# Performance work log

Measured on AMD Instinct MI355X. Metric: run time of the kernel, lower is better.

Reference implementation:

```python
import jax, jax.numpy as jnp
import numpy as np

N_NODES = 50000
N_EDGES = 800000
IN_DIM = 128
HID_DIM = 128
OUT_DIM = 128
NUM_GRAPHS = 64
NUM_CLASSES = 3


def _glorot(key, shape):
    lim = np.sqrt(6.0 / (shape[0] + shape[1])).astype(np.float32)
    return jax.random.uniform(key, shape, jnp.float32, -lim, lim)


def setup_inputs() -> dict:
    key = jax.random.key(0)
    ks = jax.random.split(key, 10)
    x = jax.random.normal(ks[0], (N_NODES, IN_DIM), jnp.float32)
    edge_index = jax.random.randint(ks[1], (2, N_EDGES), 0, N_NODES, jnp.int32).astype(jnp.int64)
    batch = jnp.sort(jax.random.randint(ks[2], (N_NODES,), 0, NUM_GRAPHS, jnp.int32)).astype(jnp.int64)
    return {
        "x": x,
        "edge_index": edge_index,
        "batch": batch,
        "W1": _glorot(ks[3], (IN_DIM, HID_DIM)),  "b1": jnp.zeros((HID_DIM,), jnp.float32),
        "W2": _glorot(ks[4], (HID_DIM, HID_DIM)), "b2": jnp.zeros((HID_DIM,), jnp.float32),
        "W3": _glorot(ks[5], (HID_DIM, OUT_DIM)), "b3": jnp.zeros((OUT_DIM,), jnp.float32),
        "C1": _glorot(ks[6], (OUT_DIM, HID_DIM)), "bc1": jnp.zeros((HID_DIM,), jnp.float32),
        "C2": _glorot(ks[7], (HID_DIM, NUM_CLASSES)), "bc2": jnp.zeros((NUM_CLASSES,), jnp.float32),
    }


def _gcn_conv(x, src, dst, norm, W, b):
    # PyG GCNConv: linear transform, then normalized gather/scatter aggregation, then bias.
    h = x @ W                               # [N, F_out]
    msg = h[src] * norm[:, None]            # [E+N, F_out] irregular gather
    return jax.ops.segment_sum(msg, dst, num_segments=N_NODES) + b


def reference(x, edge_index, batch, W1, b1, W2, b2, W3, b3, C1, bc1, C2, bc2):
    loops = jnp.arange(N_NODES, dtype=edge_index.dtype)
    src = jnp.concatenate([edge_index[0], loops])  # add self-loops as in GCNConv
    dst = jnp.concatenate([edge_index[1], loops])
    deg = jax.ops.segment_sum(jnp.ones_like(dst, jnp.float32), dst, num_segments=N_NODES)
    dinv = jnp.where(deg > 0, jax.lax.rsqrt(deg), 0.0)
    norm = dinv[src] * dinv[dst]            # symmetric D^-1/2 (A+I) D^-1/2 weights

    # dropout(p=0.2) is identity at inference time
    h = jax.nn.relu(_gcn_conv(x, src, dst, norm, W1, b1))
    h = jax.nn.relu(_gcn_conv(h, src, dst, norm, W2, b2))
    h = _gcn_conv(h, src, dst, norm, W3, b3)

    # global mean pool over batch segment ids
    counts = jax.ops.segment_sum(jnp.ones((N_NODES,), jnp.float32), batch, num_segments=NUM_GRAPHS)
    pooled = jax.ops.segment_sum(h, batch, num_segments=NUM_GRAPHS) / jnp.maximum(counts, 1.0)[:, None]

    g = jax.nn.relu(pooled @ C1 + bc1)      # classifier MLP (dropout 0.3 inactive)
    return g @ C2 + bc2                     # [NUM_GRAPHS, 3]
```

## Files before the change

kernel.cpp:

```cpp
#include <hip/hip_runtime.h>
#include <hip/hip_bf16.h>

#define N_NODES    50000
#define DIM        128
#define NUM_GRAPHS 64
#define NUM_CLASSES 3
#define NPAD       50176
#define XPITCH     136

typedef unsigned short ushort_t;
typedef unsigned int   uint_t;
typedef __attribute__((ext_vector_type(8))) short short8;
typedef __attribute__((ext_vector_type(4))) float f32x4;

__device__ __forceinline__ ushort_t f2bf(float f) {
    union { float f; uint_t u; } v; v.f = f;
    uint_t r = v.u + 0x7fffu + ((v.u >> 16) & 1u);
    return (ushort_t)(r >> 16);
}
__device__ __forceinline__ float bflo(uint_t u) {
    union { uint_t u; float f; } v; v.u = u << 16; return v.f;
}
__device__ __forceinline__ float bfhi(uint_t u) {
    union { uint_t u; float f; } v; v.u = u & 0xffff0000u; return v.f;
}

__device__ __forceinline__ void gather_raw(
    int n, int lane, const int* __restrict__ rowptr,
    const int* __restrict__ csr_src, const uint_t* __restrict__ Tb,
    float2& acc)
{
    int p0 = rowptr[n], p1 = rowptr[n + 1];
    uint_t us = Tb[n * 64 + lane];
    float2 a0 = make_float2(bflo(us), bfhi(us));
    float2 a1 = make_float2(0.f, 0.f);
    int p = p0;
    int nb = (p1 - p0) >> 3;
    if (nb > 0) {
        uint_t ucur[8];
        #pragma unroll
        for (int q = 0; q < 8; ++q) ucur[q] = Tb[csr_src[p + q] * 64 + lane];
        for (int b = 1; b < nb; ++b) {
            uint_t unxt[8];
            #pragma unroll
            for (int q = 0; q < 8; ++q) unxt[q] = Tb[csr_src[p + 8 + q] * 64 + lane];
            #pragma unroll
            for (int q = 0; q < 8; q += 2) {
                a0.x += bflo(ucur[q]);     a0.y += bfhi(ucur[q]);
                a1.x += bflo(ucur[q + 1]); a1.y += bfhi(ucur[q + 1]);
            }
            #pragma unroll
            for (int q = 0; q < 8; ++q) ucur[q] = unxt[q];
            p += 8;
        }
        #pragma unroll
        for (int q = 0; q < 8; q += 2) {
            a0.x += bflo(ucur[q]);     a0.y += bfhi(ucur[q]);
            a1.x += bflo(ucur[q + 1]); a1.y += bfhi(ucur[q + 1]);
        }
        p += 8;
    }
    for (; p + 4 <= p1; p += 4) {
        int s[4]; uint_t u[4];
        #pragma unroll
        for (int q = 0; q < 4; ++q) s[q] = csr_src[p + q];
        #pragma unroll
        for (int q = 0; q < 4; ++q) u[q] = Tb[s[q] * 64 + lane];
        #pragma unroll
        for (int q = 0; q < 4; q += 2) {
            a0.x += bflo(u[q]);     a0.y += bfhi(u[q]);
            a1.x += bflo(u[q + 1]); a1.y += bfhi(u[q + 1]);
        }
    }
    for (; p < p1; ++p) {
        int s = csr_src[p];
        uint_t u = Tb[s * 64 + lane];
        a0.x += bflo(u); a0.y += bfhi(u);
    }
    acc.x += a0.x + a1.x;
    acc.y += a0.y + a1.y;
}

__global__ void k_init(int* degi, float* pooled, float* counts) {
    int i = blockIdx.x * 256 + threadIdx.x;
    if (i < NPAD) degi[i] = 0;
    if (i < NUM_GRAPHS * DIM) pooled[i] = 0.0f;
    if (i < NUM_GRAPHS) counts[i] = 0.0f;
}

__global__ void k_prep(const float* __restrict__ W1, const float* __restrict__ W2,
                       const float* __restrict__ W3, ushort_t* __restrict__ Wt) {
    int i = blockIdx.x * 256 + threadIdx.x;
    int mat = i >> 14;
    int idx = i & 16383;
    const float* W = (mat == 0) ? W1 : (mat == 1) ? W2 : W3;
    int n = idx >> 7, k = idx & 127;
    Wt[mat * 16384 + n * 128 + k] = f2bf(W[k * 128 + n]);
}

__global__ void k_count(const int* __restrict__ dst, int* degi, int* rank, int nedges) {
    int e = blockIdx.x * 256 + threadIdx.x;
    if (e < nedges) rank[e] = atomicAdd(&degi[dst[e]], 1);
}

__global__ __launch_bounds__(256) void k_scan1(const int* __restrict__ degi,
                                               int* rowptr, int* bsum) {
    __shared__ int sh[256];
    int i = blockIdx.x * 256 + threadIdx.x;
    int v = degi[i];
    sh[threadIdx.x] = v;
    __syncthreads();
    for (int off = 1; off < 256; off <<= 1) {
        int t = (threadIdx.x >= off) ? sh[threadIdx.x - off] : 0;
        __syncthreads();
        sh[threadIdx.x] += t;
        __syncthreads();
    }
    rowptr[i] = sh[threadIdx.x] - v;
    if (threadIdx.x == 255) bsum[blockIdx.x] = sh[255];
}

__global__ __launch_bounds__(256) void k_scan2(int* bsum, int nblocks) {
    __shared__ int sh[256];
    int v = (threadIdx.x < nblocks) ? bsum[threadIdx.x] : 0;
    sh[threadIdx.x] = v;
    __syncthreads();
    for (int off = 1; off < 256; off <<= 1) {
        int t = (threadIdx.x >= off) ? sh[threadIdx.x - off] : 0;
        __syncthreads();
        sh[threadIdx.x] += t;
        __syncthreads();
    }
    if (threadIdx.x < nblocks) bsum[threadIdx.x] = sh[threadIdx.x] - v;
}

__global__ __launch_bounds__(256) void k_scan3(int* rowptr, const int* __restrict__ bsum,
                                               const int* __restrict__ degi,
                                               float* dinv) {
    int i = blockIdx.x * 256 + threadIdx.x;
    rowptr[i] = rowptr[i] + bsum[blockIdx.x];
    if (i < N_NODES) dinv[i] = rsqrtf((float)degi[i] + 1.0f);
}

__global__ void k_fill(const int* __restrict__ src, const int* __restrict__ dst,
                       const int* __restrict__ rank, const int* __restrict__ rowptr,
                       int* csr_src, int nedges) {
    int e = blockIdx.x * 256 + threadIdx.x;
    if (e < nedges) csr_src[rowptr[dst[e]] + rank[e]] = src[e];
}

__global__ __launch_bounds__(256) void k_mm1(
    const float* __restrict__ xin, const ushort_t* __restrict__ WtG,
    const float* __restrict__ dinv, ushort_t* __restrict__ TbOut)
{
    __shared__ ushort_t Wl[DIM * XPITCH];
    __shared__ ushort_t Xl[64 * XPITCH];

    const int tid = threadIdx.x;
    const int rowbase = blockIdx.x * 64;

    #pragma unroll
    for (int i = 0; i < 8; ++i) {
        int g = tid + i * 256;
        uint4 v = ((const uint4*)WtG)[g];
        *((uint4*)&Wl[(g >> 4) * XPITCH + (g & 15) * 8]) = v;
    }
    #pragma unroll
    for (int i = 0; i < 8; ++i) {
        int c = tid + i * 256;
        int row = c >> 5;
        int grow = rowbase + row;
        float4 f = make_float4(0.f, 0.f, 0.f, 0.f);
        if (grow < N_NODES)
            f = ((const float4*)xin)[(long long)rowbase * 32 + c];
        ushort4 h;
        h.x = f2bf(f.x); h.y = f2bf(f.y); h.z = f2bf(f.z); h.w = f2bf(f.w);
        *((ushort4*)&Xl[row * XPITCH + (c & 31) * 4]) = h;
    }
    __syncthreads();

    const int wave = tid >> 6;
    const int lane = tid & 63;
    const int quad = lane >> 4;
    const int lm   = lane & 15;
    const int m0   = wave * 16;

    short8 af[4];
    #pragma unroll
    for (int k0 = 0; k0 < 4; ++k0)
        af[k0] = *(const short8*)&Xl[(m0 + lm) * XPITCH + k0 * 32 + quad * 8];

    int noder[4]; float di[4]; bool okr[4];
    #pragma unroll
    for (int r = 0; r < 4; ++r) {
        noder[r] = rowbase + m0 + quad * 4 + r;
        okr[r] = (noder[r] < N_NODES);
        di[r] = okr[r] ? dinv[noder[r]] : 0.f;
    }

    for (int n0 = 0; n0 < DIM; n0 += 16) {
        f32x4 acc = {0.f, 0.f, 0.f, 0.f};
        #pragma unroll
        for (int k0 = 0; k0 < 4; ++k0) {
            short8 bf = *(const short8*)&Wl[(n0 + lm) * XPITCH + k0 * 32 + quad * 8];
            acc = __builtin_amdgcn_mfma_f32_16x16x32_bf16(af[k0], bf, acc, 0, 0, 0);
        }
        int n = n0 + lm;
        #pragma unroll
        for (int r = 0; r < 4; ++r)
            if (okr[r])
                TbOut[(long long)noder[r] * DIM + n] = f2bf(acc[r] * di[r]);
    }
}

__global__ __launch_bounds__(256) void k_fused(
    const int* __restrict__ rowptr, const int* __restrict__ csr_src,
    const float* __restrict__ dinv, const uint_t* __restrict__ TbIn,
    const ushort_t* __restrict__ WtG, const float* __restrict__ b_prev,
    ushort_t* __restrict__ TbOut)
{
    __shared__ ushort_t Xl[16 * XPITCH];

    const int tid = threadIdx.x;
    const int rowbase = blockIdx.x * 16;
    const int wave = tid >> 6;
    const int lane = tid & 63;

    float2 bias2 = ((const float2*)b_prev)[lane];

    #pragma unroll
    for (int t = 0; t < 4; ++t) {
        int r = wave * 4 + t;
        int n = rowbase + r;
        float2 acc = make_float2(0.f, 0.f);
        float dd = 0.f;
        if (n < N_NODES) {
            dd = dinv[n];
            gather_raw(n, lane, rowptr, csr_src, TbIn, acc);
        }
        ushort2 h;
        h.x = f2bf(fmaxf(bias2.x + acc.x * dd, 0.f));
        h.y = f2bf(fmaxf(bias2.y + acc.y * dd, 0.f));
        *((ushort2*)&Xl[r * XPITCH + lane * 2]) = h;
    }
    __syncthreads();

    const int quad = lane >> 4;
    const int lm   = lane & 15;

    short8 af[4];
    #pragma unroll
    for (int k0 = 0; k0 < 4; ++k0)
        af[k0] = *(const short8*)&Xl[lm * XPITCH + k0 * 32 + quad * 8];

    int noder[4]; float di[4]; bool okr[4];
    #pragma unroll
    for (int r = 0; r < 4; ++r) {
        noder[r] = rowbase + quad * 4 + r;
        okr[r] = (noder[r] < N_NODES);
        di[r] = okr[r] ? dinv[noder[r]] : 0.f;
    }

    #pragma unroll
    for (int h = 0; h < 2; ++h) {
        int n0 = wave * 32 + h * 16;
        f32x4 acc = {0.f, 0.f, 0.f, 0.f};
        #pragma unroll
        for (int k0 = 0; k0 < 4; ++k0) {
            short8 bf = *(const short8*)&WtG[(n0 + lm) * DIM + k0 * 32 + quad * 8];
            acc = __builtin_amdgcn_mfma_f32_16x16x32_bf16(af[k0], bf, acc, 0, 0, 0);
        }
        int n = n0 + lm;
        #pragma unroll
        for (int r = 0; r < 4; ++r)
            if (okr[r])
                TbOut[(long long)noder[r] * DIM + n] = f2bf(acc[r] * di[r]);
    }
}

__global__ __launch_bounds__(256) void k_poolgather(
    const int* __restrict__ rowptr, const int* __restrict__ csr_src,
    const float* __restrict__ dinv, const uint_t* __restrict__ Tb,
    const float* __restrict__ b3, const int* __restrict__ batch,
    float* pooled, float* counts)
{
    __shared__ float lp[8][DIM];
    __shared__ float lc[8];

    const int tid  = threadIdx.x;
    const int wave = tid >> 6;
    const int lane = tid & 63;
    const int blk0 = blockIdx.x * 32;

    #pragma unroll
    for (int i = 0; i < 4; ++i) ((float*)lp)[tid + i * 256] = 0.f;
    if (tid < 8) lc[tid] = 0.f;
    __syncthreads();

    const int gbase = batch[min(blk0, N_NODES - 1)];
    int n0 = blk0 + wave * 8;

    if (n0 < N_NODES) {
        int nend = min(n0 + 8, N_NODES);
        float2 bias2 = ((const float2*)b3)[lane];
        int cur = batch[n0];
        int runstart = n0;
        float2 pacc = make_float2(0.f, 0.f);

        for (int n = n0; n < nend; ++n) {
            int g = batch[n];
            if (g != cur) {
                int slot = cur - gbase;
                if (slot < 8) {
                    atomicAdd(&lp[slot][2 * lane], pacc.x);
                    atomicAdd(&lp[slot][2 * lane + 1], pacc.y);
                    if (lane == 0) atomicAdd(&lc[slot], (float)(n - runstart));
                } else {
                    atomicAdd(&pooled[cur * DIM + 2 * lane], pacc.x);
                    atomicAdd(&pooled[cur * DIM + 2 * lane + 1], pacc.y);
                    if (lane == 0) atomicAdd(&counts[cur], (float)(n - runstart));
                }
                pacc.x = 0.f; pacc.y = 0.f; cur = g; runstart = n;
            }
            float2 acc = make_float2(0.f, 0.f);
            gather_raw(n, lane, rowptr, csr_src, Tb, acc);
            float dd = dinv[n];
            pacc.x += bias2.x + acc.x * dd;
            pacc.y += bias2.y + acc.y * dd;
        }
        int slot = cur - gbase;
        if (slot < 8) {
            atomicAdd(&lp[slot][2 * lane], pacc.x);
            atomicAdd(&lp[slot][2 * lane + 1], pacc.y);
            if (lane == 0) atomicAdd(&lc[slot], (float)(nend - runstart));
        } else {
            atomicAdd(&pooled[cur * DIM + 2 * lane], pacc.x);
            atomicAdd(&pooled[cur * DIM + 2 * lane + 1], pacc.y);
            if (lane == 0) atomicAdd(&counts[cur], (float)(nend - runstart));
        }
    }
    __syncthreads();

    #pragma unroll
    for (int s = 0; s < 8; ++s) {
        if (lc[s] != 0.f) {
            if (tid < DIM) atomicAdd(&pooled[(gbase + s) * DIM + tid], lp[s][tid]);
            if (tid == DIM) atomicAdd(&counts[gbase + s], lc[s]);
        }
    }
}

__global__ __launch_bounds__(128) void k_cls(
    const float* __restrict__ pooled, const float* __restrict__ counts,
    const float* __restrict__ C1, const float* __restrict__ bc1,
    const float* __restrict__ C2, const float* __restrict__ bc2,
    float* out)
{
    __shared__ float pm[DIM];
    __shared__ float gv[DIM];
    int g = blockIdx.x, j = threadIdx.x;
    float cnt = fmaxf(counts[g], 1.0f);
    pm[j] = pooled[g * DIM + j] / cnt;
    __syncthreads();
    float a = bc1[j];
    for (int k = 0; k < DIM; ++k) a += pm[k] * C1[k * DIM + j];
    gv[j] = fmaxf(a, 0.f);
    __syncthreads();
    if (j < NUM_CLASSES) {
        float o = bc2[j];
        for (int k = 0; k < DIM; ++k) o += gv[k] * C2[k * NUM_CLASSES + j];
        out[g * NUM_CLASSES + j] = o;
    }
}

extern "C" void kernel_launch(void* const* d_in, const int* in_sizes, int n_in,
                              void* d_out, int out_size, void* d_ws, size_t ws_size,
                              hipStream_t stream) {
    const float* x    = (const float*)d_in[0];
    const int*   ei   = (const int*)d_in[1];
    const int*   batch= (const int*)d_in[2];
    const float* W1   = (const float*)d_in[3];
    const float* b1   = (const float*)d_in[4];
    const float* W2   = (const float*)d_in[5];
    const float* b2   = (const float*)d_in[6];
    const float* W3   = (const float*)d_in[7];
    const float* b3   = (const float*)d_in[8];
    const float* C1   = (const float*)d_in[9];
    const float* bc1  = (const float*)d_in[10];
    const float* C2   = (const float*)d_in[11];
    const float* bc2  = (const float*)d_in[12];

    const int nedges = in_sizes[1] / 2;
    const int* src = ei;
    const int* dst = ei + nedges;

    float*    dinv    = (float*)d_ws;
    uint_t*   TbA     = (uint_t*)(dinv + NPAD);
    uint_t*   TbB     = TbA + (long long)N_NODES * 64;
    float*    pooled  = (float*)(TbB + (long long)N_NODES * 64);
    float*    counts  = pooled + NUM_GRAPHS * DIM;
    int*      degi    = (int*)(counts + 64);
    int*      rowptr  = degi + NPAD;
    int*      bsum    = rowptr + NPAD + 256;
    int*      rank    = bsum + 256;
    int*      csr_src = rank + nedges;
    ushort_t* Wt      = (ushort_t*)(csr_src + nedges);

    const int nodeBlocks = NPAD / 256;
    const int mmBlocks   = (N_NODES + 63) / 64;
    const int fusedBlocks= (N_NODES + 15) / 16;
    const int pgBlocks   = (N_NODES + 31) / 32;
    const int edgeBlocks = (nedges + 255) / 256;

    k_init<<<nodeBlocks, 256, 0, stream>>>(degi, pooled, counts);
    k_prep<<<192, 256, 0, stream>>>(W1, W2, W3, Wt);
    k_count<<<edgeBlocks, 256, 0, stream>>>(dst, degi, rank, nedges);
    k_scan1<<<nodeBlocks, 256, 0, stream>>>(degi, rowptr, bsum);
    k_scan2<<<1, 256, 0, stream>>>(bsum, nodeBlocks);
    k_scan3<<<nodeBlocks, 256, 0, stream>>>(rowptr, bsum, degi, dinv);
    k_fill<<<edgeBlocks, 256, 0, stream>>>(src, dst, rank, rowptr, csr_src, nedges);

    k_mm1<<<mmBlocks, 256, 0, stream>>>(x, Wt, dinv, (ushort_t*)TbA);
    k_fused<<<fusedBlocks, 256, 0, stream>>>(rowptr, csr_src, dinv, TbA,
                                             Wt + 16384, b1, (ushort_t*)TbB);
    k_fused<<<fusedBlocks, 256, 0, stream>>>(rowptr, csr_src, dinv, TbB,
                                             Wt + 32768, b2, (ushort_t*)TbA);
    k_poolgather<<<pgBlocks, 256, 0, stream>>>(rowptr, csr_src, dinv, TbA,
                                               b3, batch, pooled, counts);
    k_cls<<<NUM_GRAPHS, 128, 0, stream>>>(pooled, counts, C1, bc1, C2, bc2,
                                          (float*)d_out);
}
```

Baseline: 301.5 us.

## Gather two rows per wave with 8-byte loads per lane

New measurement: 318.2 us. +5.5%, slower.

```diff
diff --git a/kernel.cpp b/kernel.cpp
--- a/kernel.cpp
+++ b/kernel.cpp
@@ -25,29 +25,31 @@
     union { uint_t u; float f; } v; v.u = u & 0xffff0000u; return v.f;
 }
 
-__device__ __forceinline__ void gather_raw(
-    int n, int lane, const int* __restrict__ rowptr,
-    const int* __restrict__ csr_src, const uint_t* __restrict__ Tb,
-    float2& acc)
+__device__ __forceinline__ void gather_row4(
+    int n, int fl, const int* __restrict__ rowptr,
+    const int* __restrict__ csr_src, const uint2* __restrict__ Tb2,
+    float4& out)
 {
-    int p0 = rowptr[n], p1 = rowptr[n + 1];
-    uint_t us = Tb[n * 64 + lane];
-    float2 a0 = make_float2(bflo(us), bfhi(us));
-    float2 a1 = make_float2(0.f, 0.f);
-    int p = p0;
-    int nb = (p1 - p0) >> 3;
-    if (nb > 0) {
-        uint_t ucur[8];
-        #pragma unroll
-        for (int q = 0; q < 8; ++q) ucur[q] = Tb[csr_src[p + q] * 64 + lane];
-        for (int b = 1; b < nb; ++b) {
-            uint_t unxt[8];
+    int p  = rowptr[n];
+    int p1 = rowptr[n + 1];
+    uint2 us = Tb2[n * 32 + fl];
+    float4 a0 = make_float4(bflo(us.x), bfhi(us.x), bflo(us.y), bfhi(us.y));
+    float4 a1 = make_float4(0.f, 0.f, 0.f, 0.f);
+    if (p + 8 <= p1) {
+        uint2 ucur[8];
+        #pragma unroll
+        for (int q = 0; q < 8; ++q) ucur[q] = Tb2[csr_src[p + q] * 32 + fl];
+        p += 8;
+        while (p + 8 <= p1) {
+            uint2 unxt[8];
             #pragma unroll
-            for (int q = 0; q < 8; ++q) unxt[q] = Tb[csr_src[p + 8 + q] * 64 + lane];
+            for (int q = 0; q < 8; ++q) unxt[q] = Tb2[csr_src[p + q] * 32 + fl];
             #pragma unroll
             for (int q = 0; q < 8; q += 2) {
-                a0.x += bflo(ucur[q]);     a0.y += bfhi(ucur[q]);
-                a1.x += bflo(ucur[q + 1]); a1.y += bfhi(ucur[q + 1]);
+                a0.x += bflo(ucur[q].x);   a0.y += bfhi(ucur[q].x);
+                a0.z += bflo(ucur[q].y);   a0.w += bfhi(ucur[q].y);
+                a1.x += bflo(ucur[q+1].x); a1.y += bfhi(ucur[q+1].x);
+                a1.z += bflo(ucur[q+1].y); a1.w += bfhi(ucur[q+1].y);
             }
             #pragma unroll
             for (int q = 0; q < 8; ++q) ucur[q] = unxt[q];
@@ -55,30 +57,29 @@
         }
         #pragma unroll
         for (int q = 0; q < 8; q += 2) {
-            a0.x += bflo(ucur[q]);     a0.y += bfhi(ucur[q]);
-            a1.x += bflo(ucur[q + 1]); a1.y += bfhi(ucur[q + 1]);
-        }
-        p += 8;
-    }
-    for (; p + 4 <= p1; p += 4) {
-        int s[4]; uint_t u[4];
-        #pragma unroll
-        for (int q = 0; q < 4; ++q) s[q] = csr_src[p + q];
-        #pragma unroll
-        for (int q = 0; q < 4; ++q) u[q] = Tb[s[q] * 64 + lane];
-        #pragma unroll
-        for (int q = 0; q < 4; q += 2) {
-            a0.x += bflo(u[q]);     a0.y += bfhi(u[q]);
-            a1.x += bflo(u[q + 1]); a1.y += bfhi(u[q + 1]);
-        }
-    }
-    for (; p < p1; ++p) {
-        int s = csr_src[p];
-        uint_t u = Tb[s * 64 + lane];
-        a0.x += bflo(u); a0.y += bfhi(u);
-    }
-    acc.x += a0.x + a1.x;
-    acc.y += a0.y + a1.y;
+            a0.x += bflo(ucur[q].x);   a0.y += bfhi(ucur[q].x);
+            a0.z += bflo(ucur[q].y);   a0.w += bfhi(ucur[q].y);
+            a1.x += bflo(ucur[q+1].x); a1.y += bfhi(ucur[q+1].x);
+            a1.z += bflo(ucur[q+1].y); a1.w += bfhi(ucur[q+1].y);
+        }
+    }
+    for (; p + 2 <= p1; p += 2) {
+        uint2 u0 = Tb2[csr_src[p] * 32 + fl];
+        uint2 u1 = Tb2[csr_src[p + 1] * 32 + fl];
+        a0.x += bflo(u0.x); a0.y += bfhi(u0.x);
+        a0.z += bflo(u0.y); a0.w += bfhi(u0.y);
+        a1.x += bflo(u1.x); a1.y += bfhi(u1.x);
+        a1.z += bflo(u1.y); a1.w += bfhi(u1.y);
+    }
+    if (p < p1) {
+        uint2 u = Tb2[csr_src[p] * 32 + fl];
+        a0.x += bflo(u.x); a0.y += bfhi(u.x);
+        a0.z += bflo(u.y); a0.w += bfhi(u.y);
+    }
+    out.x += a0.x + a1.x;
+    out.y += a0.y + a1.y;
+    out.z += a0.z + a1.z;
+    out.w += a0.w + a1.w;
 }
 
 __global__ void k_init(int* degi, float* pooled, float* counts) {
@@ -225,23 +226,28 @@
     const int rowbase = blockIdx.x * 16;
     const int wave = tid >> 6;
     const int lane = tid & 63;
-
-    float2 bias2 = ((const float2*)b_prev)[lane];
-
-    #pragma unroll
-    for (int t = 0; t < 4; ++t) {
-        int r = wave * 4 + t;
+    const int half = lane >> 5;
+    const int fl   = lane & 31;
+    const uint2* Tb2 = (const uint2*)TbIn;
+
+    float4 bias4 = ((const float4*)b_prev)[fl];
+
+    #pragma unroll
+    for (int i = 0; i < 2; ++i) {
+        int r = wave * 4 + i * 2 + half;
         int n = rowbase + r;
-        float2 acc = make_float2(0.f, 0.f);
+        float4 acc = make_float4(0.f, 0.f, 0.f, 0.f);
         float dd = 0.f;
         if (n < N_NODES) {
             dd = dinv[n];
-            gather_raw(n, lane, rowptr, csr_src, TbIn, acc);
-        }
-        ushort2 h;
-        h.x = f2bf(fmaxf(bias2.x + acc.x * dd, 0.f));
-        h.y = f2bf(fmaxf(bias2.y + acc.y * dd, 0.f));
-        *((ushort2*)&Xl[r * XPITCH + lane * 2]) = h;
+            gather_row4(n, fl, rowptr, csr_src, Tb2, acc);
+        }
+        ushort4 h4;
+        h4.x = f2bf(fmaxf(bias4.x + acc.x * dd, 0.f));
+        h4.y = f2bf(fmaxf(bias4.y + acc.y * dd, 0.f));
+        h4.z = f2bf(fmaxf(bias4.z + acc.z * dd, 0.f));
+        h4.w = f2bf(fmaxf(bias4.w + acc.w * dd, 0.f));
+        *((ushort4*)&Xl[r * XPITCH + fl * 4]) = h4;
     }
     __syncthreads();
 
@@ -290,7 +296,10 @@
     const int tid  = threadIdx.x;
     const int wave = tid >> 6;
     const int lane = tid & 63;
+    const int half = lane >> 5;
+    const int fl   = lane & 31;
     const int blk0 = blockIdx.x * 32;
+    const uint2* Tb2 = (const uint2*)Tb;
 
     #pragma unroll
     for (int i = 0; i < 4; ++i) ((float*)lp)[tid + i * 256] = 0.f;
@@ -298,45 +307,63 @@
     __syncthreads();
 
     const int gbase = batch[min(blk0, N_NODES - 1)];
-    int n0 = blk0 + wave * 8;
-
-    if (n0 < N_NODES) {
-        int nend = min(n0 + 8, N_NODES);
-        float2 bias2 = ((const float2*)b3)[lane];
-        int cur = batch[n0];
-        int runstart = n0;
-        float2 pacc = make_float2(0.f, 0.f);
-
-        for (int n = n0; n < nend; ++n) {
-            int g = batch[n];
-            if (g != cur) {
-                int slot = cur - gbase;
-                if (slot < 8) {
-                    atomicAdd(&lp[slot][2 * lane], pacc.x);
-                    atomicAdd(&lp[slot][2 * lane + 1], pacc.y);
-                    if (lane == 0) atomicAdd(&lc[slot], (float)(n - runstart));
-                } else {
-                    atomicAdd(&pooled[cur * DIM + 2 * lane], pacc.x);
-                    atomicAdd(&pooled[cur * DIM + 2 * lane + 1], pacc.y);
-                    if (lane == 0) atomicAdd(&counts[cur], (float)(n - runstart));
+    const int nbase = blk0 + wave * 8;
+    const int firstn = nbase + half;
+
+    if (firstn < N_NODES) {
+        float4 bias4 = ((const float4*)b3)[fl];
+        int cur = batch[firstn];
+        int cnt = 0;
+        float4 pacc = make_float4(0.f, 0.f, 0.f, 0.f);
+
+        #pragma unroll
+        for (int i = 0; i < 4; ++i) {
+            int n = nbase + 2 * i + half;
+            if (n < N_NODES) {
+                int g = batch[n];
+                if (g != cur) {
+                    int slot = cur - gbase;
+                    if (slot < 8) {
+                        atomicAdd(&lp[slot][4 * fl + 0], pacc.x);
+                        atomicAdd(&lp[slot][4 * fl + 1], pacc.y);
+                        atomicAdd(&lp[slot][4 * fl + 2], pacc.z);
+                        atomicAdd(&lp[slot][4 * fl + 3], pacc.w);
+                        if (fl == 0) atomicAdd(&lc[slot], (float)cnt);
+                    } else {
+                        atomicAdd(&pooled[cur * DIM + 4 * fl + 0], pacc.x);
+                        atomicAdd(&pooled[cur * DIM + 4 * fl + 1], pacc.y);
+                        atomicAdd(&pooled[cur * DIM + 4 * fl + 2], pacc.z);
+                        atomicAdd(&pooled[cur * DIM + 4 * fl + 3], pacc.w);
+                        if (fl == 0) atomicAdd(&counts[cur], (float)cnt);
+                    }
+                    pacc = make_float4(0.f, 0.f, 0.f, 0.f);
+                    cnt = 0; cur = g;
                 }
-                pacc.x = 0.f; pacc.y = 0.f; cur = g; runstart = n;
+                float4 acc = make_float4(0.f, 0.f, 0.f, 0.f);
+                gather_row4(n, fl, rowptr, csr_src, Tb2, acc);
+                float dd = dinv[n];
+                pacc.x += bias4.x + acc.x * dd;
+                pacc.y += bias4.y + acc.y * dd;
+                pacc.z += bias4.z + acc.z * dd;
+                pacc.w += bias4.w + acc.w * dd;
+                ++cnt;
             }
-            float2 acc = make_float2(0.f, 0.f);
-            gather_raw(n, lane, rowptr, csr_src, Tb, acc);
-            float dd = dinv[n];
-            pacc.x += bias2.x + acc.x * dd;
-            pacc.y += bias2.y + acc.y * dd;
-        }
-        int slot = cur - gbase;
-        if (slot < 8) {
-            atomicAdd(&lp[slot][2 * lane], pacc.x);
-            atomicAdd(&lp[slot][2 * lane + 1], pacc.y);
-            if (lane == 0) atomicAdd(&lc[slot], (float)(nend - runstart));
-        } else {
-            atomicAdd(&pooled[cur * DIM + 2 * lane], pacc.x);
-            atomicAdd(&pooled[cur * DIM + 2 * lane + 1], pacc.y);
-            if (lane == 0) atomicAdd(&counts[cur], (float)(nend - runstart));
+        }
+        if (cnt > 0) {
+            int slot = cur - gbase;
+            if (slot < 8) {
+                atomicAdd(&lp[slot][4 * fl + 0], pacc.x);
+                atomicAdd(&lp[slot][4 * fl + 1], pacc.y);
+                atomicAdd(&lp[slot][4 * fl + 2], pacc.z);
+                atomicAdd(&lp[slot][4 * fl + 3], pacc.w);
+                if (fl == 0) atomicAdd(&lc[slot], (float)cnt);
+            } else {
+                atomicAdd(&pooled[cur * DIM + 4 * fl + 0], pacc.x);
+                atomicAdd(&pooled[cur * DIM + 4 * fl + 1], pacc.y);
+                atomicAdd(&pooled[cur * DIM + 4 * fl + 2], pacc.z);
+                atomicAdd(&pooled[cur * DIM + 4 * fl + 3], pacc.w);
+                if (fl == 0) atomicAdd(&counts[cur], (float)cnt);
+            }
         }
     }
     __syncthreads();
```
